# Optimization experiments

Measured on AMD Instinct MI355X. Metric: run time of the kernel, lower is better.

## Reference

```python
import jax, jax.numpy as jnp
import numpy as np

HEADS = 4
DIM_HEAD = 32
DIM = 128
B, N, Hq, Wg = 2, 6, 32, 32   # batch, cameras, BEV grid
HK, WK = 28, 60               # image feature map


def _ln(x, g, b, eps=1e-5):
    mu = jnp.mean(x, axis=-1, keepdims=True)
    var = jnp.mean((x - mu) ** 2, axis=-1, keepdims=True)
    return (x - mu) * jax.lax.rsqrt(var + eps) * g + b


def setup_inputs() -> dict:
    key = jax.random.key(0)
    ks = jax.random.split(key, 12)
    s = 0.05  # weight scale to keep softmax logits well-conditioned
    inp = {
        'q': jax.random.normal(ks[0], (B, N, DIM, Hq, Wg), jnp.float32),
        'k': jax.random.normal(ks[1], (B, N, DIM, HK, WK), jnp.float32),
        'v': jax.random.normal(ks[2], (B, N, DIM, HK, WK), jnp.float32),
        'skip': jax.random.normal(ks[3], (B, DIM, Hq, Wg), jnp.float32),
        'q_ln_g': jnp.ones((DIM,), jnp.float32),
        'q_ln_b': jnp.zeros((DIM,), jnp.float32),
        'Wq': s * jax.random.normal(ks[4], (DIM, HEADS * DIM_HEAD), jnp.float32),
        'bq': jnp.zeros((HEADS * DIM_HEAD,), jnp.float32),
        'k_ln_g': jnp.ones((DIM,), jnp.float32),
        'k_ln_b': jnp.zeros((DIM,), jnp.float32),
        'Wk': s * jax.random.normal(ks[5], (DIM, HEADS * DIM_HEAD), jnp.float32),
        'bk': jnp.zeros((HEADS * DIM_HEAD,), jnp.float32),
        'v_ln_g': jnp.ones((DIM,), jnp.float32),
        'v_ln_b': jnp.zeros((DIM,), jnp.float32),
        'Wv': s * jax.random.normal(ks[6], (DIM, HEADS * DIM_HEAD), jnp.float32),
        'bv': jnp.zeros((HEADS * DIM_HEAD,), jnp.float32),
        'Wp': s * jax.random.normal(ks[7], (HEADS * DIM_HEAD, DIM), jnp.float32),
        'bp': jnp.zeros((DIM,), jnp.float32),
        'pre_g': jnp.ones((DIM,), jnp.float32),
        'pre_b': jnp.zeros((DIM,), jnp.float32),
        'W1': s * jax.random.normal(ks[8], (DIM, 2 * DIM), jnp.float32),
        'b1': jnp.zeros((2 * DIM,), jnp.float32),
        'W2': s * jax.random.normal(ks[9], (2 * DIM, DIM), jnp.float32),
        'b2': jnp.zeros((DIM,), jnp.float32),
        'post_g': jnp.ones((DIM,), jnp.float32),
        'post_b': jnp.zeros((DIM,), jnp.float32),
    }
    return inp


def reference(q, k, v, skip, q_ln_g, q_ln_b, Wq, bq, k_ln_g, k_ln_b, Wk, bk,
              v_ln_g, v_ln_b, Wv, bv, Wp, bp, pre_g, pre_b,
              W1, b1, W2, b2, post_g, post_b):
    b, n, d, H, W = q.shape
    Q = H * W
    K = k.shape[3] * k.shape[4]
    m, dh = HEADS, DIM_HEAD
    # b n d H W -> b n Q d   /  b n d h w -> b n K d  /  b (n K) d
    qf = q.transpose(0, 1, 3, 4, 2).reshape(b, n, Q, d)
    kf = k.transpose(0, 1, 3, 4, 2).reshape(b, n, K, d)
    vf = v.transpose(0, 1, 3, 4, 2).reshape(b, n * K, d)
    # norm -> linear, then split heads: b ... (m dh) -> (b m) ... dh
    qh = (_ln(qf, q_ln_g, q_ln_b) @ Wq + bq).reshape(b, n, Q, m, dh)
    qh = qh.transpose(0, 3, 1, 2, 4).reshape(b * m, n, Q, dh)
    kh = (_ln(kf, k_ln_g, k_ln_b) @ Wk + bk).reshape(b, n, K, m, dh)
    kh = kh.transpose(0, 3, 1, 2, 4).reshape(b * m, n, K, dh)
    vh = (_ln(vf, v_ln_g, v_ln_b) @ Wv + bv).reshape(b, n * K, m, dh)
    vh = vh.transpose(0, 2, 1, 3).reshape(b * m, n * K, dh)
    scale = dh ** -0.5
    dot = scale * jnp.einsum('anqd,ankd->anqk', qh, kh)   # (b m) n Q K
    dot = dot.transpose(0, 2, 1, 3).reshape(b * m, Q, n * K)  # fold views into keys
    att = jax.nn.softmax(dot, axis=-1)
    a = jnp.einsum('aqk,akd->aqd', att, vh)               # (b m) Q dh
    a = a.reshape(b, m, Q, dh).transpose(0, 2, 1, 3).reshape(b, Q, m * dh)
    z = a @ Wp + bp
    z = z + skip.transpose(0, 2, 3, 1).reshape(b, Q, d)
    z = _ln(z, pre_g, pre_b)
    z = z + (jax.nn.gelu(z @ W1 + b1, approximate=False) @ W2 + b2)
    z = _ln(z, post_g, post_b)
    return z.reshape(b, H, W, d).transpose(0, 3, 1, 2)
```

## Files before the change

### kernel.cpp

```cpp
#include <hip/hip_runtime.h>
#include <math.h>

#define NCAM 6
#define BSZ 2
#define SQL 1024
#define SKL 1680
#define NHEAD 4
#define DHEAD 32
#define QSCALE 0.25503494f

typedef unsigned short ushort_t;
typedef unsigned int uint_t;
typedef __attribute__((ext_vector_type(8))) short short8;
typedef __attribute__((ext_vector_type(4))) float f32x4;
typedef __attribute__((ext_vector_type(4))) uint_t uint4v;

#define MFMA16 __builtin_amdgcn_mfma_f32_16x16x32_bf16

__device__ __forceinline__ ushort_t f2bf(float x) {
  uint_t u = __builtin_bit_cast(uint_t, x);
  u += 0x7FFFu + ((u >> 16) & 1u);
  return (ushort_t)(u >> 16);
}

__device__ __forceinline__ uint_t pk2(float e0, float e1) {
  return __builtin_amdgcn_perm(__builtin_bit_cast(uint_t, e1), __builtin_bit_cast(uint_t, e0), 0x07060302u);
}

__device__ __forceinline__ float fast_gelu(float x) {
  const float ax = fabsf(x) * 0.70710678118654752f;
  const float tt = __builtin_amdgcn_rcpf(fmaf(0.3275911f, ax, 1.f));
  float poly = fmaf(tt, 1.061405429f, -1.453152027f);
  poly = fmaf(tt, poly, 1.421413741f);
  poly = fmaf(tt, poly, -0.284496736f);
  poly = fmaf(tt, poly, 0.254829592f);
  poly *= tt;
  const float e = __builtin_amdgcn_exp2f(-ax * ax * 1.4426950408889634f);
  float er = fmaf(-poly, e, 1.f);
  er = copysignf(er, x);
  return 0.5f * x * (1.f + er);
}

__global__ __launch_bounds__(256) void prep_kernel(
    const float* __restrict__ Wq, const float* __restrict__ qg, const float* __restrict__ qb, const float* __restrict__ bq,
    const float* __restrict__ Wk, const float* __restrict__ kg, const float* __restrict__ kbb, const float* __restrict__ bk,
    const float* __restrict__ Wv, const float* __restrict__ vg, const float* __restrict__ vbb, const float* __restrict__ bv,
    const float* __restrict__ Wp,
    const float* __restrict__ W1, const float* __restrict__ pre_g, const float* __restrict__ pre_b, const float* __restrict__ b1,
    const float* __restrict__ W2,
    ushort_t* WqT, ushort_t* WkT, ushort_t* WvT, ushort_t* WpT, ushort_t* W1T, ushort_t* W2T,
    float* uq, float* bbq, float* uk, float* bbk, float* uv, float* bbv, float* b1p) {
  const int mb = blockIdx.x;
  const float *W, *g = nullptr, *bln = nullptr, *bias = nullptr;
  ushort_t* WT; float *u = nullptr, *bb = nullptr;
  int kin = 128, nout = 128, ob;
  if (mb < 4)       { W=Wq; g=qg; bln=qb;   bias=bq; WT=WqT; u=uq; bb=bbq; ob=mb*32; }
  else if (mb < 8)  { W=Wk; g=kg; bln=kbb;  bias=bk; WT=WkT; u=uk; bb=bbk; ob=(mb-4)*32; }
  else if (mb < 12) { W=Wv; g=vg; bln=vbb;  bias=bv; WT=WvT; u=uv; bb=bbv; ob=(mb-8)*32; }
  else if (mb < 16) { W=Wp; WT=WpT; ob=(mb-12)*32; }
  else if (mb < 24) { W=W1; g=pre_g; bln=pre_b; bias=b1; WT=W1T; bb=b1p; nout=256; ob=(mb-16)*32; }
  else              { W=W2; WT=W2T; kin=256; ob=(mb-24)*32; }
  const int t = threadIdx.x;
  const int oc = t & 31, ig = t >> 5;
  const int out = ob + oc;
  const int nper = kin >> 3;
  float su = 0.f, sb = 0.f;
  for (int j0 = 0; j0 < nper; j0 += 8) {
    float wv8[8];
#pragma unroll
    for (int j = 0; j < 8; ++j)
      wv8[j] = W[(size_t)(ig * nper + j0 + j) * nout + out];
#pragma unroll
    for (int j = 0; j < 8; ++j) {
      const int in = ig * nper + j0 + j;
      const float wg = g ? g[in] * wv8[j] : wv8[j];
      WT[(size_t)out * kin + in] = f2bf(wg);
      su += wg;
      if (bln) sb += bln[in] * wv8[j];
    }
  }
  __shared__ float sU[8][32], sB[8][32];
  sU[ig][oc] = su; sB[ig][oc] = sb;
  __syncthreads();
  if (t < 32) {
    float tu = 0.f, tb = 0.f;
#pragma unroll
    for (int i = 0; i < 8; ++i) { tu += sU[i][t]; tb += sB[i][t]; }
    if (u)  u[ob + t] = tu;
    if (bb) bb[ob + t] = tb + (bias ? bias[ob + t] : 0.f);
  }
}

__global__ __launch_bounds__(256) void proj_mfma(
    const float* __restrict__ xq, const float* __restrict__ xk, const float* __restrict__ xv,
    const ushort_t* __restrict__ WqT, const ushort_t* __restrict__ WkT, const ushort_t* __restrict__ WvT,
    const float* __restrict__ uq, const float* __restrict__ uk, const float* __restrict__ uv,
    const float* __restrict__ bbq, const float* __restrict__ bbk, const float* __restrict__ bbv,
    ushort_t* __restrict__ Qh, ushort_t* __restrict__ Kh, ushort_t* __restrict__ Vt) {
  int blk = blockIdx.x;
  const float* x; const ushort_t* WT; const float* u; const float* bb;
  ushort_t* out; int S, ntile, vmode; float oscale;
  if (blk < 192)      { x=xq; WT=WqT; u=uq; bb=bbq; out=Qh; S=SQL; ntile=16; vmode=0; oscale=QSCALE; }
  else if (blk < 516) { blk-=192; x=xk; WT=WkT; u=uk; bb=bbk; out=Kh; S=SKL; ntile=27; vmode=0; oscale=1.f; }
  else                { blk-=516; x=xv; WT=WvT; u=uv; bb=bbv; out=Vt; S=SKL; ntile=27; vmode=1; oscale=1.f; }
  const int bn = blk / ntile;
  const int pos0 = (blk - bn * ntile) * 64;
  int valid = S - pos0; if (valid > 64) valid = 64;

  const int t = threadIdx.x;
  __shared__ ushort_t sX[64 * 128];
  __shared__ float sS1[16][64], sS2[16][64];
  __shared__ float sMu[64], sRs[64];

  {
    const int posq = t & 15, chg = t >> 4;
    int lp4 = 4 * posq; if (lp4 >= valid) lp4 = valid - 4;
    const float* xb = x + ((size_t)bn * 128 + chg * 8) * S + pos0 + lp4;
    float v[8][4];
#pragma unroll
    for (int i = 0; i < 8; ++i) {
      const float4 f = *((const float4*)(xb + (size_t)i * S));
      v[i][0] = f.x; v[i][1] = f.y; v[i][2] = f.z; v[i][3] = f.w;
    }
#pragma unroll
    for (int j = 0; j < 4; ++j) {
      float s1 = 0.f, s2 = 0.f;
#pragma unroll
      for (int i = 0; i < 8; ++i) { s1 += v[i][j]; s2 += v[i][j] * v[i][j]; }
      sS1[chg][lp4 + j] = s1; sS2[chg][lp4 + j] = s2;
    }
#pragma unroll
    for (int j = 0; j < 4; ++j) {
      const int pos = lp4 + j;
      short8 pk;
#pragma unroll
      for (int i = 0; i < 8; ++i) pk[i] = (short)f2bf(v[i][j]);
      const int phys = chg ^ (pos & 7);
      *((short8*)&sX[pos * 128 + phys * 8]) = pk;
    }
  }
  __syncthreads();
  if (t < 64) {
    float a1 = 0.f, a2 = 0.f;
#pragma unroll
    for (int g = 0; g < 16; ++g) { a1 += sS1[g][t]; a2 += sS2[g][t]; }
    const float mu = a1 * (1.f / 128.f);
    sMu[t] = mu; sRs[t] = rsqrtf(a2 * (1.f / 128.f) - mu * mu + 1e-5f);
  }
  __syncthreads();

  const int w = t >> 6, l = t & 63, lq = l & 15, quad = l >> 4;
  short8 af[2][4];
#pragma unroll
  for (int ms = 0; ms < 2; ++ms)
#pragma unroll
    for (int kk = 0; kk < 4; ++kk)
      af[ms][kk] = *((const short8*)(WT + (size_t)(w * 32 + ms * 16 + lq) * 128 + quad * 8 + kk * 32));
  f32x4 acc[4][2];
#pragma unroll
  for (int ns = 0; ns < 4; ++ns)
#pragma unroll
    for (int ms = 0; ms < 2; ++ms) acc[ns][ms] = (f32x4){0.f, 0.f, 0.f, 0.f};
#pragma unroll
  for (int ns = 0; ns < 4; ++ns) {
    short8 bf[4];
#pragma unroll
    for (int kk = 0; kk < 4; ++kk) {
      const int phys = (quad + 4 * kk) ^ (lq & 7);
      bf[kk] = *((const short8*)&sX[(ns * 16 + lq) * 128 + phys * 8]);
    }
#pragma unroll
    for (int ms = 0; ms < 2; ++ms) {
      f32x4 a = acc[ns][ms];
#pragma unroll
      for (int kk = 0; kk < 4; ++kk) a = MFMA16(af[ms][kk], bf[kk], a, 0, 0, 0);
      acc[ns][ms] = a;
    }
  }

  const int b_ = bn / NCAM, cam = bn - b_ * NCAM;
  const size_t slab = (size_t)((b_ * NHEAD + w) * NCAM + cam);
#pragma unroll
  for (int ms = 0; ms < 2; ++ms) {
    float uu[4], bv_[4];
#pragma unroll
    for (int r = 0; r < 4; ++r) {
      const int og = w * 32 + ms * 16 + quad * 4 + r;
      uu[r] = u[og]; bv_[r] = bb[og];
    }
#pragma unroll
    for (int ns = 0; ns < 4; ++ns) {
      const int p = ns * 16 + lq;
      if (p < valid) {
        const float mu = sMu[p], rs = sRs[p];
        float val[4];
#pragma unroll
        for (int r = 0; r < 4; ++r)
          val[r] = ((acc[ns][ms][r] - mu * uu[r]) * rs + bv_[r]) * oscale;
        if (vmode == 0) {
          ushort_t e0 = f2bf(val[0]), e1 = f2bf(val[1]), e2 = f2bf(val[2]), e3 = f2bf(val[3]);
          ushort_t* orow = out + (slab * S + pos0 + p) * 32 + ms * 16 + quad * 4;
          *((uint_t*)orow) = (uint_t)e0 | ((uint_t)e1 << 16);
          *((uint_t*)(orow + 2)) = (uint_t)e2 | ((uint_t)e3 << 16);
        } else {
#pragma unroll
          for (int r = 0; r < 4; ++r)
            out[(slab * 32 + ms * 16 + quad * 4 + r) * (size_t)SKL + pos0 + p] = f2bf(val[r]);
        }
      }
    }
  }
}

__global__ __launch_bounds__(512, 2) void attn_mfma(
    const ushort_t* __restrict__ Qh, const ushort_t* __restrict__ Kh,
    const ushort_t* __restrict__ Vt, ushort_t* __restrict__ Ab) {
  const int t = threadIdx.x;
  const int w = t >> 6, l = t & 63;
  const int lq = l & 15, quad = l >> 4;
  const int bm = blockIdx.x & 7;
  const int q0 = (blockIdx.x >> 3) * 32;
  const int camg = w >> 2, kq = w & 3;
  const int kstart = kq * 448;
  const int nfull = (kq == 3) ? 5 : 7;

  __shared__ __align__(16) unsigned char smem[74752];
  float (*sO)[2][16][36] = (float(*)[2][16][36])smem;
  float (*sL)[2][16] = (float(*)[2][16])(smem + 73728);

  f32x4 oA0 = {0.f,0.f,0.f,0.f}, oA1 = {0.f,0.f,0.f,0.f};
  f32x4 oB0 = {0.f,0.f,0.f,0.f}, oB1 = {0.f,0.f,0.f,0.f};
  float lA = 0.f, lB = 0.f;

  for (int nc = 0; nc < 3; ++nc) {
    const int n = camg * 3 + nc;
    const ushort_t* Kb = Kh + (size_t)(bm * NCAM + n) * SKL * 32;
    const ushort_t* Vb = Vt + (size_t)(bm * NCAM + n) * 32 * SKL;
    const ushort_t* Qbase = Qh + ((size_t)(bm * NCAM + n) * SQL + q0) * 32;
    const short8 qfA = *((const short8*)(Qbase + (size_t)lq * 32 + quad * 8));
    const short8 qfB = *((const short8*)(Qbase + (size_t)(16 + lq) * 32 + quad * 8));

    short8 kc[4];
#pragma unroll
    for (int st = 0; st < 4; ++st)
      kc[st] = *((const short8*)(Kb + (size_t)(kstart + st * 16 + lq) * 32 + quad * 8));

    for (int kt = 0; kt < nfull; ++kt) {
      const int kb = kstart + kt * 64;
      const int vq = quad * 4;
      const ushort_t* vp0 = Vb + (size_t)lq * SKL + kb + vq;
      const ushort_t* vp1 = Vb + (size_t)(16 + lq) * SKL + kb + vq;
      const uint2 r00 = *((const uint2*)(vp0));
      const uint2 r01 = *((const uint2*)(vp0 + 16));
      const uint2 r02 = *((const uint2*)(vp0 + 32));
      const uint2 r03 = *((const uint2*)(vp0 + 48));
      const uint2 r10 = *((const uint2*)(vp1));
      const uint2 r11 = *((const uint2*)(vp1 + 16));
      const uint2 r12 = *((const uint2*)(vp1 + 32));
      const uint2 r13 = *((const uint2*)(vp1 + 48));
      uint4v c;
      c[0] = r00.x; c[1] = r00.y; c[2] = r01.x; c[3] = r01.y;
      const short8 v00 = __builtin_bit_cast(short8, c);
      c[0] = r02.x; c[1] = r02.y; c[2] = r03.x; c[3] = r03.y;
      const short8 v01 = __builtin_bit_cast(short8, c);
      c[0] = r10.x; c[1] = r10.y; c[2] = r11.x; c[3] = r11.y;
      const short8 v10 = __builtin_bit_cast(short8, c);
      c[0] = r12.x; c[1] = r12.y; c[2] = r13.x; c[3] = r13.y;
      const short8 v11 = __builtin_bit_cast(short8, c);
      short8 kn[4] = {kc[0], kc[1], kc[2], kc[3]};
      if (kt + 1 < nfull) {
        const int kbn = kb + 64;
#pragma unroll
        for (int st = 0; st < 4; ++st)
          kn[st] = *((const short8*)(Kb + (size_t)(kbn + st * 16 + lq) * 32 + quad * 8));
      }

      f32x4 sA[4], sB[4];
#pragma unroll
      for (int st = 0; st < 4; ++st) {
        f32x4 z = {0.f, 0.f, 0.f, 0.f};
        sA[st] = MFMA16(kc[st], qfA, z, 0, 0, 0);
        sB[st] = MFMA16(kc[st], qfB, z, 0, 0, 0);
      }
      float eA[4][4], eB[4][4];
#pragma unroll
      for (int st = 0; st < 4; ++st) {
#pragma unroll
        for (int r = 0; r < 4; ++r) {
          eA[st][r] = __builtin_amdgcn_exp2f(sA[st][r]);
          eB[st][r] = __builtin_amdgcn_exp2f(sB[st][r]);
        }
        lA += (eA[st][0] + eA[st][1]) + (eA[st][2] + eA[st][3]);
        lB += (eB[st][0] + eB[st][1]) + (eB[st][2] + eB[st][3]);
      }
      uint4v pw;
      pw[0] = pk2(eA[0][0], eA[0][1]); pw[1] = pk2(eA[0][2], eA[0][3]);
      pw[2] = pk2(eA[1][0], eA[1][1]); pw[3] = pk2(eA[1][2], eA[1][3]);
      const short8 pfA0 = __builtin_bit_cast(short8, pw);
      pw[0] = pk2(eA[2][0], eA[2][1]); pw[1] = pk2(eA[2][2], eA[2][3]);
      pw[2] = pk2(eA[3][0], eA[3][1]); pw[3] = pk2(eA[3][2], eA[3][3]);
      const short8 pfA1 = __builtin_bit_cast(short8, pw);
      pw[0] = pk2(eB[0][0], eB[0][1]); pw[1] = pk2(eB[0][2], eB[0][3]);
      pw[2] = pk2(eB[1][0], eB[1][1]); pw[3] = pk2(eB[1][2], eB[1][3]);
      const short8 pfB0 = __builtin_bit_cast(short8, pw);
      pw[0] = pk2(eB[2][0], eB[2][1]); pw[1] = pk2(eB[2][2], eB[2][3]);
      pw[2] = pk2(eB[3][0], eB[3][1]); pw[3] = pk2(eB[3][2], eB[3][3]);
      const short8 pfB1 = __builtin_bit_cast(short8, pw);

      oA0 = MFMA16(v00, pfA0, oA0, 0, 0, 0);
      oA1 = MFMA16(v10, pfA0, oA1, 0, 0, 0);
      oB0 = MFMA16(v00, pfB0, oB0, 0, 0, 0);
      oB1 = MFMA16(v10, pfB0, oB1, 0, 0, 0);
      oA0 = MFMA16(v01, pfA1, oA0, 0, 0, 0);
      oA1 = MFMA16(v11, pfA1, oA1, 0, 0, 0);
      oB0 = MFMA16(v01, pfB1, oB0, 0, 0, 0);
      oB1 = MFMA16(v11, pfB1, oB1, 0, 0, 0);
#pragma unroll
      for (int st = 0; st < 4; ++st) kc[st] = kn[st];
    }

    if (kq == 3) {
      const int kb = kstart + 320;
      const int vq = quad * 4;
      const short8 kf = *((const short8*)(Kb + (size_t)(kb + lq) * 32 + quad * 8));
      const uint2 r00 = *((const uint2*)(Vb + (size_t)lq * SKL + kb + vq));
      const uint2 r10 = *((const uint2*)(Vb + (size_t)(16 + lq) * SKL + kb + vq));
      uint4v c;
      c[0] = r00.x; c[1] = r00.y; c[2] = 0u; c[3] = 0u;
      const short8 v00 = __builtin_bit_cast(short8, c);
      c[0] = r10.x; c[1] = r10.y; c[2] = 0u; c[3] = 0u;
      const short8 v10 = __builtin_bit_cast(short8, c);
      f32x4 z = {0.f, 0.f, 0.f, 0.f};
      const f32x4 s0A = MFMA16(kf, qfA, z, 0, 0, 0);
      const f32x4 s0B = MFMA16(kf, qfB, z, 0, 0, 0);
      float eA[4], eB[4];
#pragma unroll
      for (int r = 0; r < 4; ++r) {
        eA[r] = __builtin_amdgcn_exp2f(s0A[r]);
        eB[r] = __builtin_amdgcn_exp2f(s0B[r]);
      }
      lA += (eA[0] + eA[1]) + (eA[2] + eA[3]);
      lB += (eB[0] + eB[1]) + (eB[2] + eB[3]);
      uint4v pw;
      pw[0] = pk2(eA[0], eA[1]); pw[1] = pk2(eA[2], eA[3]); pw[2] = 0u; pw[3] = 0u;
      const short8 pfA0 = __builtin_bit_cast(short8, pw);
      pw[0] = pk2(eB[0], eB[1]); pw[1] = pk2(eB[2], eB[3]); pw[2] = 0u; pw[3] = 0u;
      const short8 pfB0 = __builtin_bit_cast(short8, pw);
      oA0 = MFMA16(v00, pfA0, oA0, 0, 0, 0);
      oA1 = MFMA16(v10, pfA0, oA1, 0, 0, 0);
      oB0 = MFMA16(v00, pfB0, oB0, 0, 0, 0);
      oB1 = MFMA16(v10, pfB0, oB1, 0, 0, 0);
    }
  }

  lA += __shfl_xor(lA, 16, 64);
  lA += __shfl_xor(lA, 32, 64);
  lB += __shfl_xor(lB, 16, 64);
  lB += __shfl_xor(lB, 32, 64);

  *((f32x4*)&sO[w][0][lq][quad * 4]) = oA0;
  *((f32x4*)&sO[w][0][lq][16 + quad * 4]) = oA1;
  *((f32x4*)&sO[w][1][lq][quad * 4]) = oB0;
  *((f32x4*)&sO[w][1][lq][16 + quad * 4]) = oB1;
  if (l < 16) { sL[w][0][l] = lA; sL[w][1][l] = lB; }
  __syncthreads();
  if (w < 2) {
    const int frag = w;
    float lf = 0.f;
    f32x4 a0 = {0.f, 0.f, 0.f, 0.f}, a1 = {0.f, 0.f, 0.f, 0.f};
#pragma unroll
    for (int ww = 0; ww < 8; ++ww) {
      lf += sL[ww][frag][lq];
      a0 += *((const f32x4*)&sO[ww][frag][lq][quad * 4]);
      a1 += *((const f32x4*)&sO[ww][frag][lq][16 + quad * 4]);
    }
    const float inv = 1.f / lf;
    const int b = bm >> 2, hm = bm & 3;
    ushort_t* op = Ab + ((size_t)b * SQL + q0 + frag * 16 + lq) * 128 + hm * 32 + quad * 4;
    ushort4 w0 = make_ushort4(f2bf(a0[0] * inv), f2bf(a0[1] * inv), f2bf(a0[2] * inv), f2bf(a0[3] * inv));
    ushort4 w1 = make_ushort4(f2bf(a1[0] * inv), f2bf(a1[1] * inv), f2bf(a1[2] * inv), f2bf(a1[3] * inv));
    *((ushort4*)op) = w0;
    *((ushort4*)(op + 16)) = w1;
  }
}

__global__ __launch_bounds__(256) void post_mfma(
    const ushort_t* __restrict__ Ab, const float* __restrict__ skip,
    const ushort_t* __restrict__ WpT, const float* __restrict__ bp,
    const float* __restrict__ pre_g, const float* __restrict__ pre_b,
    const ushort_t* __restrict__ W1T, const float* __restrict__ b1p,
    const ushort_t* __restrict__ W2T, const float* __restrict__ b2,
    const float* __restrict__ post_g, const float* __restrict__ post_b,
    float* __restrict__ out) {
  const int t = threadIdx.x;
  const int w = t >> 6, l = t & 63, lq = l & 15, quad = l >> 4;
  const int b = blockIdx.x >> 7;
  const int p0 = (blockIdx.x & 127) * 8;
  const int rp = (p0 + lq < SQL) ? (p0 + lq) : (SQL - 1);

  __shared__ float zf[16 * 132];
  __shared__ float sRes[16 * 132];
  __shared__ ushort_t sZb[16 * 128];
  __shared__ ushort_t sH[16 * 256];
  __shared__ float sMu[16], sRs[16];

  f32x4 z[2] = {{0.f,0.f,0.f,0.f},{0.f,0.f,0.f,0.f}};
#pragma unroll
  for (int kk = 0; kk < 4; ++kk) {
    const short8 bfr = *((const short8*)(Ab + ((size_t)b * SQL + rp) * 128 + quad * 8 + kk * 32));
#pragma unroll
    for (int ms = 0; ms < 2; ++ms) {
      const short8 afr = *((const short8*)(WpT + (size_t)(w * 32 + ms * 16 + lq) * 128 + quad * 8 + kk * 32));
      z[ms] = MFMA16(afr, bfr, z[ms], 0, 0, 0);
    }
  }
#pragma unroll
  for (int ms = 0; ms < 2; ++ms)
#pragma unroll
    for (int r = 0; r < 4; ++r) {
      const int o = w * 32 + ms * 16 + quad * 4 + r;
      const int rr = (p0 + lq < SQL) ? (p0 + lq) : (SQL - 1);
      zf[lq * 132 + o] = z[ms][r] + bp[o] + skip[(size_t)b * 131072 + (size_t)o * 1024 + rr];
    }
  __syncthreads();
  {
    const int pos = t >> 4, j = t & 15;
    float s1 = 0.f, s2 = 0.f;
#pragma unroll
    for (int c = 0; c < 8; ++c) { const float vv = zf[pos * 132 + j * 8 + c]; s1 += vv; s2 += vv * vv; }
    s1 += __shfl_xor(s1, 1, 64); s1 += __shfl_xor(s1, 2, 64);
    s1 += __shfl_xor(s1, 4, 64); s1 += __shfl_xor(s1, 8, 64);
    s2 += __shfl_xor(s2, 1, 64); s2 += __shfl_xor(s2, 2, 64);
    s2 += __shfl_xor(s2, 4, 64); s2 += __shfl_xor(s2, 8, 64);
    if (j == 0) {
      const float mu = s1 * (1.f / 128.f);
      sMu[pos] = mu; sRs[pos] = rsqrtf(s2 * (1.f / 128.f) - mu * mu + 1e-5f);
    }
  }
  __syncthreads();
  {
    const int pos = t & 15, grp = t >> 4;
    const float mu = sMu[pos], rs = sRs[pos];
    short8 pk;
#pragma unroll
    for (int i = 0; i < 8; ++i) {
      const int ch = grp * 8 + i;
      const float nv = (zf[pos * 132 + ch] - mu) * rs;
      pk[i] = (short)f2bf(nv);
      sRes[pos * 132 + ch] = nv * pre_g[ch] + pre_b[ch];
    }
    *((short8*)&sZb[pos * 128 + (grp ^ (pos & 7)) * 8]) = pk;
  }
  __syncthreads();
  f32x4 h[4];
#pragma unroll
  for (int ms = 0; ms < 4; ++ms) h[ms] = (f32x4){0.f, 0.f, 0.f, 0.f};
  short8 bz[4];
#pragma unroll
  for (int kk = 0; kk < 4; ++kk)
    bz[kk] = *((const short8*)&sZb[lq * 128 + ((quad + 4 * kk) ^ (lq & 7)) * 8]);
#pragma unroll
  for (int ms = 0; ms < 4; ++ms)
#pragma unroll
    for (int kk = 0; kk < 4; ++kk) {
      const short8 afr = *((const short8*)(W1T + (size_t)(w * 64 + ms * 16 + lq) * 128 + quad * 8 + kk * 32));
      h[ms] = MFMA16(afr, bz[kk], h[ms], 0, 0, 0);
    }
#pragma unroll
  for (int ms = 0; ms < 4; ++ms)
#pragma unroll
    for (int r = 0; r < 4; ++r) {
      const int o = w * 64 + ms * 16 + quad * 4 + r;
      const float hv = fast_gelu(h[ms][r] + b1p[o]);
      const int phys = (o >> 3) ^ (lq & 7);
      sH[lq * 256 + phys * 8 + (o & 7)] = f2bf(hv);
    }
  __syncthreads();
  f32x4 z2[2] = {{0.f,0.f,0.f,0.f},{0.f,0.f,0.f,0.f}};
#pragma unroll
  for (int kk = 0; kk < 8; ++kk) {
    const short8 bh = *((const short8*)&sH[lq * 256 + ((quad + 4 * kk) ^ (lq & 7)) * 8]);
#pragma unroll
    for (int ms = 0; ms < 2; ++ms) {
      const short8 afr = *((const short8*)(W2T + (size_t)(w * 32 + ms * 16 + lq) * 256 + quad * 8 + kk * 32));
      z2[ms] = MFMA16(afr, bh, z2[ms], 0, 0, 0);
    }
  }
  __syncthreads();
#pragma unroll
  for (int ms = 0; ms < 2; ++ms)
#pragma unroll
    for (int r = 0; r < 4; ++r) {
      const int o = w * 32 + ms * 16 + quad * 4 + r;
      zf[lq * 132 + o] = z2[ms][r] + b2[o] + sRes[lq * 132 + o];
    }
  __syncthreads();
  {
    const int pos = t >> 4, j = t & 15;
    float s1 = 0.f, s2 = 0.f;
#pragma unroll
    for (int c = 0; c < 8; ++c) { const float vv = zf[pos * 132 + j * 8 + c]; s1 += vv; s2 += vv * vv; }
    s1 += __shfl_xor(s1, 1, 64); s1 += __shfl_xor(s1, 2, 64);
    s1 += __shfl_xor(s1, 4, 64); s1 += __shfl_xor(s1, 8, 64);
    s2 += __shfl_xor(s2, 1, 64); s2 += __shfl_xor(s2, 2, 64);
    s2 += __shfl_xor(s2, 4, 64); s2 += __shfl_xor(s2, 8, 64);
    if (j == 0) {
      const float mu = s1 * (1.f / 128.f);
      sMu[pos] = mu; sRs[pos] = rsqrtf(s2 * (1.f / 128.f) - mu * mu + 1e-5f);
    }
  }
  __syncthreads();
  {
    const int pos = t & 15, grp = t >> 4;
    if (pos < 8) {
      const float mu = sMu[pos], rs = sRs[pos];
#pragma unroll
      for (int i = 0; i < 8; ++i) {
        const int ch = grp * 8 + i;
        out[(size_t)b * 131072 + (size_t)ch * 1024 + p0 + pos] =
            (zf[pos * 132 + ch] - mu) * rs * post_g[ch] + post_b[ch];
      }
    }
  }
}

extern "C" void kernel_launch(void* const* d_in, const int* in_sizes, int n_in,
                              void* d_out, int out_size, void* d_ws, size_t ws_size,
                              hipStream_t stream) {
  const float* q_in   = (const float*)d_in[0];
  const float* k_in   = (const float*)d_in[1];
  const float* v_in   = (const float*)d_in[2];
  const float* skip   = (const float*)d_in[3];
  const float* q_ln_g = (const float*)d_in[4];
  const float* q_ln_b = (const float*)d_in[5];
  const float* Wq     = (const float*)d_in[6];
  const float* bq     = (const float*)d_in[7];
  const float* k_ln_g = (const float*)d_in[8];
  const float* k_ln_b = (const float*)d_in[9];
  const float* Wk     = (const float*)d_in[10];
  const float* bk     = (const float*)d_in[11];
  const float* v_ln_g = (const float*)d_in[12];
  const float* v_ln_b = (const float*)d_in[13];
  const float* Wv     = (const float*)d_in[14];
  const float* bv     = (const float*)d_in[15];
  const float* Wp     = (const float*)d_in[16];
  const float* bp     = (const float*)d_in[17];
  const float* pre_g  = (const float*)d_in[18];
  const float* pre_b  = (const float*)d_in[19];
  const float* W1     = (const float*)d_in[20];
  const float* b1     = (const float*)d_in[21];
  const float* W2     = (const float*)d_in[22];
  const float* b2     = (const float*)d_in[23];
  const float* post_g = (const float*)d_in[24];
  const float* post_b = (const float*)d_in[25];

  char* base = (char*)d_ws;
  ushort_t* WqT = (ushort_t*)base; base += 16384 * 2;
  ushort_t* WkT = (ushort_t*)base; base += 16384 * 2;
  ushort_t* WvT = (ushort_t*)base; base += 16384 * 2;
  ushort_t* WpT = (ushort_t*)base; base += 16384 * 2;
  ushort_t* W1T = (ushort_t*)base; base += 32768 * 2;
  ushort_t* W2T = (ushort_t*)base; base += 32768 * 2;
  float* uq  = (float*)base; base += 128 * 4;
  float* bbq = (float*)base; base += 128 * 4;
  float* uk  = (float*)base; base += 128 * 4;
  float* bbk = (float*)base; base += 128 * 4;
  float* uv  = (float*)base; base += 128 * 4;
  float* bbv = (float*)base; base += 128 * 4;
  float* b1p = (float*)base; base += 256 * 4;
  base = (char*)(((size_t)base + 255) & ~(size_t)255);
  ushort_t* Qh = (ushort_t*)base; base += (size_t)1572864 * 2;
  ushort_t* Kh = (ushort_t*)base; base += (size_t)(2580480 + 4096) * 2;
  ushort_t* Vt = (ushort_t*)base; base += (size_t)(2580480 + 4096) * 2;
  ushort_t* Ab = (ushort_t*)base; base += (size_t)262144 * 2;
  float* out = (float*)d_out;

  prep_kernel<<<28, 256, 0, stream>>>(
      Wq, q_ln_g, q_ln_b, bq, Wk, k_ln_g, k_ln_b, bk, Wv, v_ln_g, v_ln_b, bv,
      Wp, W1, pre_g, pre_b, b1, W2,
      WqT, WkT, WvT, WpT, W1T, W2T, uq, bbq, uk, bbk, uv, bbv, b1p);
  proj_mfma<<<840, 256, 0, stream>>>(
      q_in, k_in, v_in, WqT, WkT, WvT, uq, uk, uv, bbq, bbk, bbv, Qh, Kh, Vt);
  attn_mfma<<<256, 512, 0, stream>>>(Qh, Kh, Vt, Ab);
  post_mfma<<<256, 256, 0, stream>>>(
      Ab, skip, WpT, bp, pre_g, pre_b, W1T, b1p, W2T, b2, post_g, post_b, out);
}
```

Measured before the change: 176.5 us.

## Store V transposed in padded permuted layout for single 16-byte MFMA operand loads

The V projection epilogue now writes V^T with a padded row stride and a within-32-key permutation. This lets the attention kernel load each V MFMA operand with one 16-byte vector load instead of four 8-byte loads plus register shuffles. Padding keys are written as zeros so the tail tile reads valid data. The QK/exp/PV inner loop is also split into two half-tiles, which can lower live registers and interleave the exp work with MFMAs. The cost is slightly more workspace and scattered 2-byte stores in the projection epilogue.

```diff
diff --git a/kernel.cpp b/kernel.cpp
--- a/kernel.cpp
+++ b/kernel.cpp
@@ -5,6 +5,7 @@
 #define BSZ 2
 #define SQL 1024
 #define SKL 1680
+#define SKLP 1696
 #define NHEAD 4
 #define DHEAD 32
 #define QSCALE 0.25503494f
@@ -191,21 +192,33 @@
 #pragma unroll
     for (int ns = 0; ns < 4; ++ns) {
       const int p = ns * 16 + lq;
-      if (p < valid) {
-        const float mu = sMu[p], rs = sRs[p];
-        float val[4];
-#pragma unroll
-        for (int r = 0; r < 4; ++r)
-          val[r] = ((acc[ns][ms][r] - mu * uu[r]) * rs + bv_[r]) * oscale;
-        if (vmode == 0) {
+      if (vmode == 0) {
+        if (p < valid) {
+          const float mu = sMu[p], rs = sRs[p];
+          float val[4];
+#pragma unroll
+          for (int r = 0; r < 4; ++r)
+            val[r] = ((acc[ns][ms][r] - mu * uu[r]) * rs + bv_[r]) * oscale;
           ushort_t e0 = f2bf(val[0]), e1 = f2bf(val[1]), e2 = f2bf(val[2]), e3 = f2bf(val[3]);
           ushort_t* orow = out + (slab * S + pos0 + p) * 32 + ms * 16 + quad * 4;
           *((uint_t*)orow) = (uint_t)e0 | ((uint_t)e1 << 16);
           *((uint_t*)(orow + 2)) = (uint_t)e2 | ((uint_t)e3 << 16);
-        } else {
+        }
+      } else {
+        const int key = pos0 + p;
+        if (key < SKLP) {
+          ushort_t wv[4] = {0, 0, 0, 0};
+          if (p < valid) {
+            const float mu = sMu[p], rs = sRs[p];
+#pragma unroll
+            for (int r = 0; r < 4; ++r)
+              wv[r] = f2bf((acc[ns][ms][r] - mu * uu[r]) * rs + bv_[r]);
+          }
+          const int o = key & 31;
+          const int col = (key & ~31) + ((o >> 2) & 3) * 8 + ((o >> 4) << 2) + (o & 3);
 #pragma unroll
           for (int r = 0; r < 4; ++r)
-            out[(slab * 32 + ms * 16 + quad * 4 + r) * (size_t)SKL + pos0 + p] = f2bf(val[r]);
+            out[(slab * 32 + ms * 16 + quad * 4 + r) * (size_t)SKLP + col] = wv[r];
         }
       }
     }
@@ -235,7 +248,7 @@
   for (int nc = 0; nc < 3; ++nc) {
     const int n = camg * 3 + nc;
     const ushort_t* Kb = Kh + (size_t)(bm * NCAM + n) * SKL * 32;
-    const ushort_t* Vb = Vt + (size_t)(bm * NCAM + n) * 32 * SKL;
+    const ushort_t* Vb = Vt + (size_t)(bm * NCAM + n) * 32 * SKLP;
     const ushort_t* Qbase = Qh + ((size_t)(bm * NCAM + n) * SQL + q0) * 32;
     const short8 qfA = *((const short8*)(Qbase + (size_t)lq * 32 + quad * 8));
     const short8 qfB = *((const short8*)(Qbase + (size_t)(16 + lq) * 32 + quad * 8));
@@ -247,26 +260,10 @@
 
     for (int kt = 0; kt < nfull; ++kt) {
       const int kb = kstart + kt * 64;
-      const int vq = quad * 4;
-      const ushort_t* vp0 = Vb + (size_t)lq * SKL + kb + vq;
-      const ushort_t* vp1 = Vb + (size_t)(16 + lq) * SKL + kb + vq;
-      const uint2 r00 = *((const uint2*)(vp0));
-      const uint2 r01 = *((const uint2*)(vp0 + 16));
-      const uint2 r02 = *((const uint2*)(vp0 + 32));
-      const uint2 r03 = *((const uint2*)(vp0 + 48));
-      const uint2 r10 = *((const uint2*)(vp1));
-      const uint2 r11 = *((const uint2*)(vp1 + 16));
-      const uint2 r12 = *((const uint2*)(vp1 + 32));
-      const uint2 r13 = *((const uint2*)(vp1 + 48));
-      uint4v c;
-      c[0] = r00.x; c[1] = r00.y; c[2] = r01.x; c[3] = r01.y;
-      const short8 v00 = __builtin_bit_cast(short8, c);
-      c[0] = r02.x; c[1] = r02.y; c[2] = r03.x; c[3] = r03.y;
-      const short8 v01 = __builtin_bit_cast(short8, c);
-      c[0] = r10.x; c[1] = r10.y; c[2] = r11.x; c[3] = r11.y;
-      const short8 v10 = __builtin_bit_cast(short8, c);
-      c[0] = r12.x; c[1] = r12.y; c[2] = r13.x; c[3] = r13.y;
-      const short8 v11 = __builtin_bit_cast(short8, c);
+      const short8 v00 = *((const short8*)(Vb + (size_t)lq * SKLP + kb + quad * 8));
+      const short8 v01 = *((const short8*)(Vb + (size_t)lq * SKLP + kb + 32 + quad * 8));
+      const short8 v10 = *((const short8*)(Vb + (size_t)(16 + lq) * SKLP + kb + quad * 8));
+      const short8 v11 = *((const short8*)(Vb + (size_t)(16 + lq) * SKLP + kb + 32 + quad * 8));
       short8 kn[4] = {kc[0], kc[1], kc[2], kc[3]};
       if (kt + 1 < nfull) {
         const int kbn = kb + 64;
@@ -275,64 +272,73 @@
           kn[st] = *((const short8*)(Kb + (size_t)(kbn + st * 16 + lq) * 32 + quad * 8));
       }
 
-      f32x4 sA[4], sB[4];
-#pragma unroll
-      for (int st = 0; st < 4; ++st) {
-        f32x4 z = {0.f, 0.f, 0.f, 0.f};
-        sA[st] = MFMA16(kc[st], qfA, z, 0, 0, 0);
-        sB[st] = MFMA16(kc[st], qfB, z, 0, 0, 0);
+      const f32x4 zz = {0.f, 0.f, 0.f, 0.f};
+      {
+        const f32x4 s0A = MFMA16(kc[0], qfA, zz, 0, 0, 0);
+        const f32x4 s1A = MFMA16(kc[1], qfA, zz, 0, 0, 0);
+        const f32x4 s0B = MFMA16(kc[0], qfB, zz, 0, 0, 0);
+        const f32x4 s1B = MFMA16(kc[1], qfB, zz, 0, 0, 0);
+        float e0A[4], e1A[4], e0B[4], e1B[4];
+#pragma unroll
+        for (int r = 0; r < 4; ++r) {
+          e0A[r] = __builtin_amdgcn_exp2f(s0A[r]);
+          e1A[r] = __builtin_amdgcn_exp2f(s1A[r]);
+          e0B[r] = __builtin_amdgcn_exp2f(s0B[r]);
+          e1B[r] = __builtin_amdgcn_exp2f(s1B[r]);
+        }
+        lA += ((e0A[0] + e0A[1]) + (e0A[2] + e0A[3])) + ((e1A[0] + e1A[1]) + (e1A[2] + e1A[3]));
+        lB += ((e0B[0] + e0B[1]) + (e0B[2] + e0B[3])) + ((e1B[0] + e1B[1]) + (e1B[2] + e1B[3]));
+        uint4v pw;
+        pw[0] = pk2(e0A[0], e0A[1]); pw[1] = pk2(e0A[2], e0A[3]);
+        pw[2] = pk2(e1A[0], e1A[1]); pw[3] = pk2(e1A[2], e1A[3]);
+        const short8 pfA0 = __builtin_bit_cast(short8, pw);
+        pw[0] = pk2(e0B[0], e0B[1]); pw[1] = pk2(e0B[2], e0B[3]);
+        pw[2] = pk2(e1B[0], e1B[1]); pw[3] = pk2(e1B[2], e1B[3]);
+        const short8 pfB0 = __builtin_bit_cast(short8, pw);
+        oA0 = MFMA16(v00, pfA0, oA0, 0, 0, 0);
+        oA1 = MFMA16(v10, pfA0, oA1, 0, 0, 0);
+        oB0 = MFMA16(v00, pfB0, oB0, 0, 0, 0);
+        oB1 = MFMA16(v10, pfB0, oB1, 0, 0, 0);
       }
-      float eA[4][4], eB[4][4];
-#pragma unroll
-      for (int st = 0; st < 4; ++st) {
+      {
+        const f32x4 s2A = MFMA16(kc[2], qfA, zz, 0, 0, 0);
+        const f32x4 s3A = MFMA16(kc[3], qfA, zz, 0, 0, 0);
+        const f32x4 s2B = MFMA16(kc[2], qfB, zz, 0, 0, 0);
+        const f32x4 s3B = MFMA16(kc[3], qfB, zz, 0, 0, 0);
+        float e2A[4], e3A[4], e2B[4], e3B[4];
 #pragma unroll
         for (int r = 0; r < 4; ++r) {
-          eA[st][r] = __builtin_amdgcn_exp2f(sA[st][r]);
-          eB[st][r] = __builtin_amdgcn_exp2f(sB[st][r]);
+          e2A[r] = __builtin_amdgcn_exp2f(s2A[r]);
+          e3A[r] = __builtin_amdgcn_exp2f(s3A[r]);
+          e2B[r] = __builtin_amdgcn_exp2f(s2B[r]);
+          e3B[r] = __builtin_amdgcn_exp2f(s3B[r]);
         }
-        lA += (eA[st][0] + eA[st][1]) + (eA[st][2] + eA[st][3]);
-        lB += (eB[st][0] + eB[st][1]) + (eB[st][2] + eB[st][3]);
+        lA += ((e2A[0] + e2A[1]) + (e2A[2] + e2A[3])) + ((e3A[0] + e3A[1]) + (e3A[2] + e3A[3]));
+        lB += ((e2B[0] + e2B[1]) + (e2B[2] + e2B[3])) + ((e3B[0] + e3B[1]) + (e3B[2] + e3B[3]));
+        uint4v pw;
+        pw[0] = pk2(e2A[0], e2A[1]); pw[1] = pk2(e2A[2], e2A[3]);
+        pw[2] = pk2(e3A[0], e3A[1]); pw[3] = pk2(e3A[2], e3A[3]);
+        const short8 pfA1 = __builtin_bit_cast(short8, pw);
+        pw[0] = pk2(e2B[0], e2B[1]); pw[1] = pk2(e2B[2], e2B[3]);
+        pw[2] = pk2(e3B[0], e3B[1]); pw[3] = pk2(e3B[2], e3B[3]);
+        const short8 pfB1 = __builtin_bit_cast(short8, pw);
+        oA0 = MFMA16(v01, pfA1, oA0, 0, 0, 0);
+        oA1 = MFMA16(v11, pfA1, oA1, 0, 0, 0);
+        oB0 = MFMA16(v01, pfB1, oB0, 0, 0, 0);
+        oB1 = MFMA16(v11, pfB1, oB1, 0, 0, 0);
       }
-      uint4v pw;
-      pw[0] = pk2(eA[0][0], eA[0][1]); pw[1] = pk2(eA[0][2], eA[0][3]);
-      pw[2] = pk2(eA[1][0], eA[1][1]); pw[3] = pk2(eA[1][2], eA[1][3]);
-      const short8 pfA0 = __builtin_bit_cast(short8, pw);
-      pw[0] = pk2(eA[2][0], eA[2][1]); pw[1] = pk2(eA[2][2], eA[2][3]);
-      pw[2] = pk2(eA[3][0], eA[3][1]); pw[3] = pk2(eA[3][2], eA[3][3]);
-      const short8 pfA1 = __builtin_bit_cast(short8, pw);
-      pw[0] = pk2(eB[0][0], eB[0][1]); pw[1] = pk2(eB[0][2], eB[0][3]);
-      pw[2] = pk2(eB[1][0], eB[1][1]); pw[3] = pk2(eB[1][2], eB[1][3]);
-      const short8 pfB0 = __builtin_bit_cast(short8, pw);
-      pw[0] = pk2(eB[2][0], eB[2][1]); pw[1] = pk2(eB[2][2], eB[2][3]);
-      pw[2] = pk2(eB[3][0], eB[3][1]); pw[3] = pk2(eB[3][2], eB[3][3]);
-      const short8 pfB1 = __builtin_bit_cast(short8, pw);
-
-      oA0 = MFMA16(v00, pfA0, oA0, 0, 0, 0);
-      oA1 = MFMA16(v10, pfA0, oA1, 0, 0, 0);
-      oB0 = MFMA16(v00, pfB0, oB0, 0, 0, 0);
-      oB1 = MFMA16(v10, pfB0, oB1, 0, 0, 0);
-      oA0 = MFMA16(v01, pfA1, oA0, 0, 0, 0);
-      oA1 = MFMA16(v11, pfA1, oA1, 0, 0, 0);
-      oB0 = MFMA16(v01, pfB1, oB0, 0, 0, 0);
-      oB1 = MFMA16(v11, pfB1, oB1, 0, 0, 0);
 #pragma unroll
       for (int st = 0; st < 4; ++st) kc[st] = kn[st];
     }
 
     if (kq == 3) {
       const int kb = kstart + 320;
-      const int vq = quad * 4;
       const short8 kf = *((const short8*)(Kb + (size_t)(kb + lq) * 32 + quad * 8));
-      const uint2 r00 = *((const uint2*)(Vb + (size_t)lq * SKL + kb + vq));
-      const uint2 r10 = *((const uint2*)(Vb + (size_t)(16 + lq) * SKL + kb + vq));
-      uint4v c;
-      c[0] = r00.x; c[1] = r00.y; c[2] = 0u; c[3] = 0u;
-      const short8 v00 = __builtin_bit_cast(short8, c);
-      c[0] = r10.x; c[1] = r10.y; c[2] = 0u; c[3] = 0u;
-      const short8 v10 = __builtin_bit_cast(short8, c);
-      f32x4 z = {0.f, 0.f, 0.f, 0.f};
-      const f32x4 s0A = MFMA16(kf, qfA, z, 0, 0, 0);
-      const f32x4 s0B = MFMA16(kf, qfB, z, 0, 0, 0);
+      const short8 v00 = *((const short8*)(Vb + (size_t)lq * SKLP + kb + quad * 8));
+      const short8 v10 = *((const short8*)(Vb + (size_t)(16 + lq) * SKLP + kb + quad * 8));
+      const f32x4 zz = {0.f, 0.f, 0.f, 0.f};
+      const f32x4 s0A = MFMA16(kf, qfA, zz, 0, 0, 0);
+      const f32x4 s0B = MFMA16(kf, qfB, zz, 0, 0, 0);
       float eA[4], eB[4];
 #pragma unroll
       for (int r = 0; r < 4; ++r) {
@@ -571,7 +577,7 @@
   base = (char*)(((size_t)base + 255) & ~(size_t)255);
   ushort_t* Qh = (ushort_t*)base; base += (size_t)1572864 * 2;
   ushort_t* Kh = (ushort_t*)base; base += (size_t)(2580480 + 4096) * 2;
-  ushort_t* Vt = (ushort_t*)base; base += (size_t)(2580480 + 4096) * 2;
+  ushort_t* Vt = (ushort_t*)base; base += (size_t)(2605056 + 4096) * 2;
   ushort_t* Ab = (ushort_t*)base; base += (size_t)262144 * 2;
   float* out = (float*)d_out;
 
```

After: 165.3 us. 1.07x faster.
